# Performance work log

Hardware: AMD Instinct MI355X
Metric: run time of the kernel (lower is better)

The kernel has to match this reference:

```python
import jax, jax.numpy as jnp
import numpy as np

D_MODEL = 1024
N_HEADS = 16
D_HEAD = 64
NEG = -1000000000.0


def setup_inputs() -> dict:
    key = jax.random.key(0)
    k1, k2, k3 = jax.random.split(key, 3)
    B, T = 2, 2048
    x = jax.random.normal(k1, (B, T, D_MODEL), dtype=jnp.float32)
    # qkv_proj: Linear(d_model, 3*H*D, bias=False) -> weight (3*H*D, d_model)
    w_qkv = jax.random.normal(k2, (3 * N_HEADS * D_HEAD, D_MODEL), dtype=jnp.float32) * (D_MODEL ** -0.5)
    # o_proj: Linear(H*D, d_model, bias=False) -> weight (d_model, H*D)
    w_o = jax.random.normal(k3, (D_MODEL, N_HEADS * D_HEAD), dtype=jnp.float32) * ((N_HEADS * D_HEAD) ** -0.5)
    return {"x": x, "w_qkv": w_qkv, "w_o": w_o}


def reference(x, w_qkv, w_o):
    B, T, _ = x.shape
    H, D = N_HEADS, D_HEAD
    scale = D ** -0.5
    qkv = jnp.einsum('btm,nm->btn', x, w_qkv).reshape(B, T, 3, H, D)
    q, k, v = qkv[:, :, 0], qkv[:, :, 1], qkv[:, :, 2]  # (B,T,H,D)
    # scores: (B,H,T,T)
    attn = jnp.einsum('bqhd,bkhd->bhqk', q, k) * scale
    causal = jnp.tril(jnp.ones((T, T), dtype=x.dtype))
    attn = attn + (1.0 - causal) * NEG
    attn = jax.nn.softmax(attn, axis=-1)
    out = jnp.einsum('bhqk,bkhd->bqhd', attn, v).reshape(B, T, H * D)
    out = jnp.einsum('btn,mn->btm', out, w_o)
    return (out, k, v)
```

## Files before the change

kernel.cpp:

```cpp
#include <hip/hip_runtime.h>
#include <cstdint>

typedef unsigned short u16;
typedef __bf16 bf16x8 __attribute__((ext_vector_type(8)));
typedef float f32x4 __attribute__((ext_vector_type(4)));
typedef short s4 __attribute__((ext_vector_type(4)));

#define T_SEQ 2048
#define NH 16

__device__ __forceinline__ u16 f2bf(float f) {
  union { float f; uint32_t u; } x; x.f = f;
  uint32_t r = (x.u + 0x7fffu + ((x.u >> 16) & 1u)) >> 16;
  return (u16)r;
}

__device__ __forceinline__ uint32_t pk2bf(float a, float b) {
  union { float f; uint32_t u; } x, y; x.f = a; y.f = b;
  uint32_t lo = (x.u + 0x7fffu + ((x.u >> 16) & 1u)) >> 16;
  uint32_t hi = (y.u + 0x7fffu + ((y.u >> 16) & 1u)) >> 16;
  return lo | (hi << 16);
}

__device__ __forceinline__ void cvt8(u16* dst, const float* src) {
  float4 a = *(const float4*)src;
  float4 b = *(const float4*)(src + 4);
  uint4 o;
  o.x = pk2bf(a.x, a.y); o.y = pk2bf(a.z, a.w);
  o.z = pk2bf(b.x, b.y); o.w = pk2bf(b.z, b.w);
  *(uint4*)dst = o;
}

__global__ __launch_bounds__(256) void cvt_all(const float* __restrict__ x,
                                               const float* __restrict__ wq,
                                               const float* __restrict__ wo,
                                               u16* __restrict__ dst) {
  int i = blockIdx.x * 256 + threadIdx.x;
  const float* src; int off;
  if (i < 524288)      { src = x;  off = 0; }
  else if (i < 917504) { src = wq; off = 524288; }
  else                 { src = wo; off = 917504; }
  cvt8(&dst[(size_t)i * 8], &src[(size_t)(i - off) * 8]);
}

__device__ __forceinline__ s4 cvt4(f32x4 v) {
  union { __bf16 b[4]; s4 s; } u;
  u.b[0] = (__bf16)v[0]; u.b[1] = (__bf16)v[1];
  u.b[2] = (__bf16)v[2]; u.b[3] = (__bf16)v[3];
  return u.s;
}

__device__ __forceinline__ f32x4 mfma16(s4 a, s4 b, f32x4 c) {
#if __has_builtin(__builtin_amdgcn_mfma_f32_16x16x16bf16_1k)
  return __builtin_amdgcn_mfma_f32_16x16x16bf16_1k(a, b, c, 0, 0, 0);
#else
  asm("v_mfma_f32_16x16x16_bf16 %0, %1, %2, %0" : "+v"(c) : "v"(a), "v"(b));
  return c;
#endif
}

__device__ __forceinline__ float exp2fast(float x) {
#if __has_builtin(__builtin_amdgcn_exp2f)
  return __builtin_amdgcn_exp2f(x);
#else
  float r; asm("v_exp_f32 %0, %1" : "=v"(r) : "v"(x)); return r;
#endif
}

__device__ __forceinline__ void gl_lds(const u16* g, u16* ldsbase) {
  __builtin_amdgcn_global_load_lds(
      (const __attribute__((address_space(1))) void*)g,
      (__attribute__((address_space(3))) void*)ldsbase, 16, 0, 0);
}

template <bool CF32, bool KV, int BM>
__global__ __launch_bounds__(512) void gemm_bt(
    const u16* __restrict__ A, const u16* __restrict__ W,
    void* __restrict__ Cp, float* __restrict__ outk, float* __restrict__ outv,
    u16* __restrict__ vtp, int M, int N, int K) {
  constexpr int WM = BM / 2;
  constexpr int MI = WM / 16;
  constexpr int NJ = 2;
  __shared__ __align__(16) u16 As[2][BM * 64];
  __shared__ __align__(16) u16 Bs[2][128 * 64];
  const int tid  = threadIdx.x;
  const int bid  = blockIdx.y * gridDim.x + blockIdx.x;
  const int per  = (gridDim.x * gridDim.y) >> 3;
  const int swz  = (bid & 7) * per + (bid >> 3);
  const int n0   = (swz % gridDim.x) * 128;
  const int m0   = (swz / gridDim.x) * BM;
  const int lane = tid & 63;
  const int wave = tid >> 6;
  const int wm   = (wave >> 2) * WM;
  const int wn   = (wave & 3) * 32;
  const int l15  = lane & 15;
  const int quad = lane >> 4;
  const int srow = lane >> 3;
  const int sc   = lane & 7;

  f32x4 acc[MI][NJ];
#pragma unroll
  for (int i = 0; i < MI; i++)
#pragma unroll
    for (int j = 0; j < NJ; j++) acc[i][j] = (f32x4){0.f, 0.f, 0.f, 0.f};

  auto stage = [&](int d, int k0) {
#pragma unroll
    for (int i = 0; i < BM / 64; i++) {
      int r0  = (i * 8 + wave) * 8;
      int row = r0 + srow;
      int gc  = (sc ^ (row & 7)) << 3;
      gl_lds(&A[(size_t)(m0 + row) * K + k0 + gc], &As[d][r0 * 64]);
    }
#pragma unroll
    for (int i = 0; i < 2; i++) {
      int r0  = (i * 8 + wave) * 8;
      int row = r0 + srow;
      int gc  = (sc ^ (row & 7)) << 3;
      gl_lds(&W[(size_t)(n0 + row) * K + k0 + gc], &Bs[d][r0 * 64]);
    }
  };

  stage(0, 0);
  asm volatile("s_waitcnt vmcnt(0)" ::: "memory");
  __builtin_amdgcn_s_barrier();
  __builtin_amdgcn_sched_barrier(0);

  const int NT = K >> 6;
  int cur = 0;
  for (int t = 0; t < NT; t++) {
    if (t + 1 < NT) stage(cur ^ 1, (t + 1) * 64);
#pragma unroll
    for (int kk = 0; kk < 64; kk += 32) {
      bf16x8 af[MI], bfr[NJ];
#pragma unroll
      for (int i = 0; i < MI; i++) {
        int arow = wm + i * 16 + l15;
        af[i] = *(const bf16x8*)((const char*)&As[cur][0] + arow * 128 +
                                 ((((kk >> 3) + quad) ^ (arow & 7)) << 4));
      }
#pragma unroll
      for (int j = 0; j < NJ; j++) {
        int brow = wn + j * 16 + l15;
        bfr[j] = *(const bf16x8*)((const char*)&Bs[cur][0] + brow * 128 +
                                  ((((kk >> 3) + quad) ^ (brow & 7)) << 4));
      }
#pragma unroll
      for (int i = 0; i < MI; i++)
#pragma unroll
        for (int j = 0; j < NJ; j++)
          acc[i][j] = __builtin_amdgcn_mfma_f32_16x16x32_bf16(af[i], bfr[j], acc[i][j], 0, 0, 0);
    }
    asm volatile("s_waitcnt vmcnt(0)" ::: "memory");
    __builtin_amdgcn_s_barrier();
    __builtin_amdgcn_sched_barrier(0);
    cur ^= 1;
  }
#pragma unroll
  for (int i = 0; i < MI; i++)
#pragma unroll
    for (int j = 0; j < NJ; j++) {
      const int row0 = m0 + wm + i * 16 + quad * 4;
      const int col  = n0 + wn + j * 16 + l15;
      if constexpr (CF32) {
#pragma unroll
        for (int r = 0; r < 4; r++)
          ((float*)Cp)[(size_t)(row0 + r) * N + col] = acc[i][j][r];
      } else if (KV && col >= 2048) {
        const int hd = col - 2048;
        const int b_ = row0 >> 11, t_ = row0 & 2047;
        uint2 pk;
        pk.x = pk2bf(acc[i][j][0], acc[i][j][1]);
        pk.y = pk2bf(acc[i][j][2], acc[i][j][3]);
        *(uint2*)&vtp[((size_t)(b_ * NH + (hd >> 6)) * 64 + (hd & 63)) * 2048 + t_] = pk;
#pragma unroll
        for (int r = 0; r < 4; r++)
          outv[(size_t)(row0 + r) * 1024 + hd] = acc[i][j][r];
      } else {
#pragma unroll
        for (int r = 0; r < 4; r++) {
          float v = acc[i][j][r];
          ((u16*)Cp)[(size_t)(row0 + r) * N + col] = f2bf(v);
          if constexpr (KV) {
            if (col >= 1024) outk[(size_t)(row0 + r) * 1024 + (col - 1024)] = v;
          }
        }
      }
    }
}

__global__ __launch_bounds__(256) void attn(const u16* __restrict__ qkv,
                                            const u16* __restrict__ vt,
                                            u16* __restrict__ o) {
  __shared__ __align__(16) u16 Ks[2][64 * 64];
  __shared__ __align__(16) u16 Vts[2][64 * 64];

  const int tid  = threadIdx.x;
  const int bx   = blockIdx.x;
  const int by   = blockIdx.y;
  const int b    = by >> 4, h = by & 15;
  const int lane = tid & 63, wave = tid >> 6;
  const int l15  = lane & 15, quad = lane >> 4;
  const int srow = lane >> 3, sc = lane & 7;
  const size_t qbase = (size_t)b * T_SEQ * 3072;
  const size_t vbase = (size_t)(b * NH + h) * 64 * 2048;
  const float C = 0.1803368801f;

  const int u  = (bx + (by & 7) * 5) & 31;
  const int c  = by >> 3;
  const int v_ = (u + ((c >> 1) << 4)) & 31;
  const int qt = (c & 1) ? (31 - v_) : v_;
  const int steps = qt + 1;

  const int wq0  = qt * 64 + wave * 16;
  const int qrow = wq0 + l15;

  const u16* qp = &qkv[qbase + (size_t)qrow * 3072 + h * 64];
  const bf16x8 qf0 = *(const bf16x8*)&qp[quad * 8];
  const bf16x8 qf1 = *(const bf16x8*)&qp[32 + quad * 8];

  f32x4 acc_o[4];
#pragma unroll
  for (int n = 0; n < 4; n++) acc_o[n] = (f32x4){0.f, 0.f, 0.f, 0.f};
  float m2run = -1e30f, lrun = 0.f;

  auto stage = [&](int buf, int kt) {
    const int k0 = kt * 64;
#pragma unroll
    for (int i = 0; i < 2; i++) {
      int r0  = (wave * 2 + i) * 8;
      int row = r0 + srow;
      int gc  = (sc ^ (row & 7)) << 3;
      gl_lds(&qkv[qbase + (size_t)(k0 + row) * 3072 + 1024 + h * 64 + gc], &Ks[buf][r0 * 64]);
      gl_lds(&vt[vbase + (size_t)row * 2048 + k0 + gc], &Vts[buf][r0 * 64]);
    }
  };

  stage(0, 0);

  for (int s = 0; s < steps; s++) {
    const int cur = s & 1;
    asm volatile("s_waitcnt vmcnt(0)" ::: "memory");
    __builtin_amdgcn_s_barrier();
    __builtin_amdgcn_sched_barrier(0);

    if (s + 1 < steps) stage(cur ^ 1, s + 1);

    const int k0 = s * 64;

    f32x4 sacc[4];
#pragma unroll
    for (int j = 0; j < 4; j++) sacc[j] = (f32x4){0.f, 0.f, 0.f, 0.f};
    __builtin_amdgcn_s_setprio(1);
#pragma unroll
    for (int j = 0; j < 4; j++) {
      int krow = j * 16 + l15;
      const char* kb = (const char*)&Ks[cur][0] + krow * 128;
      bf16x8 kfa = *(const bf16x8*)(kb + ((quad ^ (krow & 7)) << 4));
      bf16x8 kfb = *(const bf16x8*)(kb + (((4 + quad) ^ (krow & 7)) << 4));
      sacc[j] = __builtin_amdgcn_mfma_f32_16x16x32_bf16(kfa, qf0, sacc[j], 0, 0, 0);
      sacc[j] = __builtin_amdgcn_mfma_f32_16x16x32_bf16(kfb, qf1, sacc[j], 0, 0, 0);
    }
    __builtin_amdgcn_s_setprio(0);

    if (s == qt) {
#pragma unroll
      for (int j = 0; j < 4; j++)
#pragma unroll
        for (int r = 0; r < 4; r++) {
          int k = k0 + j * 16 + quad * 4 + r;
          if (k > qrow) sacc[j][r] = -1e30f;
        }
    }

    float mj[4];
#pragma unroll
    for (int j = 0; j < 4; j++)
      mj[j] = fmaxf(fmaxf(sacc[j][0], sacc[j][1]), fmaxf(sacc[j][2], sacc[j][3]));
    float mx = fmaxf(fmaxf(mj[0], mj[1]), fmaxf(mj[2], mj[3]));
    mx = fmaxf(mx, __shfl_xor(mx, 16));
    mx = fmaxf(mx, __shfl_xor(mx, 32));
    const float m2x = mx * C;

    if (!__all(m2x <= m2run + 8.0f)) {
      const float m2new = fmaxf(m2run, m2x);
      const float alpha = exp2fast(m2run - m2new);
      lrun *= alpha;
      m2run = m2new;
#pragma unroll
      for (int r = 0; r < 4; r++) {
        float ar = __shfl(alpha, quad * 4 + r);
#pragma unroll
        for (int n = 0; n < 4; n++) acc_o[n][r] *= ar;
      }
    }

    const float nm = m2run;
    float ts[4];
#pragma unroll
    for (int j = 0; j < 4; j++) {
#pragma unroll
      for (int r = 0; r < 4; r++) sacc[j][r] = exp2fast(fmaf(sacc[j][r], C, -nm));
      ts[j] = (sacc[j][0] + sacc[j][1]) + (sacc[j][2] + sacc[j][3]);
    }
    float sum = (ts[0] + ts[1]) + (ts[2] + ts[3]);
    sum += __shfl_xor(sum, 16);
    sum += __shfl_xor(sum, 32);
    lrun += sum;

    s4 pa[4];
#pragma unroll
    for (int j = 0; j < 4; j++) pa[j] = cvt4(sacc[j]);

    __builtin_amdgcn_s_setprio(1);
#pragma unroll
    for (int j = 0; j < 4; j++)
#pragma unroll
      for (int n = 0; n < 4; n++) {
        int vrow = n * 16 + l15;
        int ch = (j * 2 + (quad >> 1)) ^ (vrow & 7);
        const s4 vf = *(const s4*)((const char*)&Vts[cur][0] + vrow * 128 +
                                   (ch << 4) + ((quad & 1) << 3));
        acc_o[n] = mfma16(pa[j], vf, acc_o[n]);
      }
    __builtin_amdgcn_s_setprio(0);
  }

  const float linv = 1.0f / lrun;
#pragma unroll
  for (int r = 0; r < 4; r++) {
    const float lr = __shfl(linv, quad * 4 + r);
    const int row = wq0 + quad * 4 + r;
#pragma unroll
    for (int n = 0; n < 4; n++)
      o[(size_t)(b * T_SEQ + row) * 1024 + h * 64 + n * 16 + l15] =
          f2bf(acc_o[n][r] * lr);
  }
}

extern "C" void kernel_launch(void* const* d_in, const int* in_sizes, int n_in,
                              void* d_out, int out_size, void* d_ws, size_t ws_size,
                              hipStream_t stream) {
  const float* x     = (const float*)d_in[0];
  const float* w_qkv = (const float*)d_in[1];
  const float* w_o   = (const float*)d_in[2];
  float* out  = (float*)d_out;
  float* outk = out + (size_t)4194304;
  float* outv = out + (size_t)8388608;

  u16* qkv = (u16*)d_ws;
  u16* vt  = qkv + (size_t)4096 * 3072;
  u16* ao  = vt  + (size_t)4194304;
  u16* xb  = ao  + (size_t)4194304;
  u16* wqb = xb  + (size_t)4194304;
  u16* wob = wqb + (size_t)3145728;

  cvt_all<<<4096, 256, 0, stream>>>(x, w_qkv, w_o, xb);

  gemm_bt<false, true, 128><<<dim3(24, 32), 512, 0, stream>>>(
      xb, wqb, qkv, outk, outv, vt, 4096, 3072, 1024);
  attn<<<dim3(32, 32), 256, 0, stream>>>(qkv, vt, ao);
  gemm_bt<true, false, 64><<<dim3(8, 64), 512, 0, stream>>>(
      ao, wob, out, nullptr, nullptr, nullptr, 4096, 1024, 1024);
}
```

Baseline: 192.9 us.

## Split causal attention KV loop across two blocks by tile parity and merge

Each query tile with qt>=1 is now processed by two blocks, one handling even KV tiles and one odd, doubling the grid to 63x32. Each block writes an unnormalized bf16 partial output plus running max and sum into scratch reused from the output buffer and the xb workspace. A new merge kernel combines the two partials with softmax rescaling. This aims to shorten the longest per-block critical path and improve load balance and occupancy, at the cost of an extra kernel launch, extra global traffic, and bf16 rounding of the partials.

After: 202.6 us. 5.0% more time.

```diff
diff --git a/kernel.cpp b/kernel.cpp
--- a/kernel.cpp
+++ b/kernel.cpp
@@ -8,11 +8,19 @@
 
 #define T_SEQ 2048
 #define NH 16
+#define P_TILES 992
+#define P_O_U16 (P_TILES * 4096)
+#define P_ML_OFF_F 2031616
+#define P_ML 128
 
 __device__ __forceinline__ u16 f2bf(float f) {
   union { float f; uint32_t u; } x; x.f = f;
   uint32_t r = (x.u + 0x7fffu + ((x.u >> 16) & 1u)) >> 16;
   return (u16)r;
+}
+
+__device__ __forceinline__ float bf2f(u16 b) {
+  union { uint32_t u; float f; } x; x.u = ((uint32_t)b) << 16; return x.f;
 }
 
 __device__ __forceinline__ uint32_t pk2bf(float a, float b) {
@@ -191,7 +199,9 @@
 
 __global__ __launch_bounds__(256) void attn(const u16* __restrict__ qkv,
                                             const u16* __restrict__ vt,
-                                            u16* __restrict__ o) {
+                                            u16* __restrict__ o,
+                                            u16* __restrict__ poA,
+                                            u16* __restrict__ poB) {
   __shared__ __align__(16) u16 Ks[2][64 * 64];
   __shared__ __align__(16) u16 Vts[2][64 * 64];
 
@@ -206,11 +216,11 @@
   const size_t vbase = (size_t)(b * NH + h) * 64 * 2048;
   const float C = 0.1803368801f;
 
-  const int u  = (bx + (by & 7) * 5) & 31;
-  const int c  = by >> 3;
-  const int v_ = (u + ((c >> 1) << 4)) & 31;
-  const int qt = (c & 1) ? (31 - v_) : v_;
-  const int steps = qt + 1;
+  int qt, parity;
+  if (bx == 62) { qt = 0; parity = 0; }
+  else          { qt = 31 - (bx >> 1); parity = bx & 1; }
+  const int nsteps = (parity == 0) ? (qt / 2 + 1) : ((qt + 1) / 2);
+  const bool split = (qt >= 1);
 
   const int wq0  = qt * 64 + wave * 16;
   const int qrow = wq0 + l15;
@@ -236,17 +246,18 @@
     }
   };
 
-  stage(0, 0);
-
-  for (int s = 0; s < steps; s++) {
+  stage(0, parity);
+
+  for (int s = 0; s < nsteps; s++) {
     const int cur = s & 1;
+    const int kt  = parity + 2 * s;
     asm volatile("s_waitcnt vmcnt(0)" ::: "memory");
     __builtin_amdgcn_s_barrier();
     __builtin_amdgcn_sched_barrier(0);
 
-    if (s + 1 < steps) stage(cur ^ 1, s + 1);
-
-    const int k0 = s * 64;
+    if (s + 1 < nsteps) stage(cur ^ 1, parity + 2 * (s + 1));
+
+    const int k0 = kt * 64;
 
     f32x4 sacc[4];
 #pragma unroll
@@ -263,7 +274,7 @@
     }
     __builtin_amdgcn_s_setprio(0);
 
-    if (s == qt) {
+    if (kt == qt) {
 #pragma unroll
       for (int j = 0; j < 4; j++)
 #pragma unroll
@@ -326,16 +337,73 @@
     __builtin_amdgcn_s_setprio(0);
   }
 
-  const float linv = 1.0f / lrun;
-#pragma unroll
-  for (int r = 0; r < 4; r++) {
-    const float lr = __shfl(linv, quad * 4 + r);
-    const int row = wq0 + quad * 4 + r;
-#pragma unroll
-    for (int n = 0; n < 4; n++)
-      o[(size_t)(b * T_SEQ + row) * 1024 + h * 64 + n * 16 + l15] =
-          f2bf(acc_o[n][r] * lr);
+  if (split) {
+    const int t = by * 31 + (qt - 1);
+    u16* po   = (parity == 0) ? poA : poB;
+    float* ml = (float*)((parity == 0) ? poA : poB) + P_ML_OFF_F;
+    u16* PO   = po + (size_t)t * 4096;
+    float* ML = ml + (size_t)t * P_ML;
+#pragma unroll
+    for (int r = 0; r < 4; r++) {
+      int row = wave * 16 + quad * 4 + r;
+#pragma unroll
+      for (int n = 0; n < 4; n++)
+        PO[row * 64 + n * 16 + l15] = f2bf(acc_o[n][r]);
+    }
+    if (quad == 0) {
+      int row = wave * 16 + l15;
+      ML[row * 2]     = m2run;
+      ML[row * 2 + 1] = lrun;
+    }
+  } else {
+    const float linv = 1.0f / lrun;
+#pragma unroll
+    for (int r = 0; r < 4; r++) {
+      const float lr = __shfl(linv, quad * 4 + r);
+      const int row = wq0 + quad * 4 + r;
+#pragma unroll
+      for (int n = 0; n < 4; n++)
+        o[(size_t)(b * T_SEQ + row) * 1024 + h * 64 + n * 16 + l15] =
+            f2bf(acc_o[n][r] * lr);
+    }
   }
+}
+
+__global__ __launch_bounds__(256) void merge_attn(const u16* __restrict__ poA,
+                                                  const u16* __restrict__ poB,
+                                                  u16* __restrict__ ao) {
+  const int qt = blockIdx.x + 1;
+  const int by = blockIdx.y;
+  const int b  = by >> 4, h = by & 15;
+  const int t  = by * 31 + (qt - 1);
+  const int tid = threadIdx.x;
+  const int row = tid >> 2;
+  const int cg  = (tid & 3) * 16;
+  const u16* POA = poA + (size_t)t * 4096 + row * 64 + cg;
+  const u16* POB = poB + (size_t)t * 4096 + row * 64 + cg;
+  const float* MLA = (const float*)poA + P_ML_OFF_F + (size_t)t * P_ML + row * 2;
+  const float* MLB = (const float*)poB + P_ML_OFF_F + (size_t)t * P_ML + row * 2;
+  const float mA = MLA[0], lA = MLA[1];
+  const float mB = MLB[0], lB = MLB[1];
+  const float m  = fmaxf(mA, mB);
+  const float sA = exp2fast(mA - m), sB = exp2fast(mB - m);
+  const float inv = 1.0f / (lA * sA + lB * sB);
+  const float fA = sA * inv, fB = sB * inv;
+  union { uint4 v[2]; u16 s[16]; } A, B;
+  A.v[0] = *(const uint4*)POA;  A.v[1] = *(const uint4*)(POA + 8);
+  B.v[0] = *(const uint4*)POB;  B.v[1] = *(const uint4*)(POB + 8);
+  float c[16];
+#pragma unroll
+  for (int k = 0; k < 16; k++)
+    c[k] = bf2f(A.s[k]) * fA + bf2f(B.s[k]) * fB;
+  uint4 o0, o1;
+  o0.x = pk2bf(c[0], c[1]);   o0.y = pk2bf(c[2], c[3]);
+  o0.z = pk2bf(c[4], c[5]);   o0.w = pk2bf(c[6], c[7]);
+  o1.x = pk2bf(c[8], c[9]);   o1.y = pk2bf(c[10], c[11]);
+  o1.z = pk2bf(c[12], c[13]); o1.w = pk2bf(c[14], c[15]);
+  u16* dst = &ao[((size_t)(b * T_SEQ + qt * 64 + row)) * 1024 + h * 64 + cg];
+  *(uint4*)dst = o0;
+  *(uint4*)(dst + 8) = o1;
 }
 
 extern "C" void kernel_launch(void* const* d_in, const int* in_sizes, int n_in,
@@ -355,11 +423,15 @@
   u16* wqb = xb  + (size_t)4194304;
   u16* wob = wqb + (size_t)3145728;
 
+  u16* poA = (u16*)out;
+  u16* poB = xb;
+
   cvt_all<<<4096, 256, 0, stream>>>(x, w_qkv, w_o, xb);
 
   gemm_bt<false, true, 128><<<dim3(24, 32), 512, 0, stream>>>(
       xb, wqb, qkv, outk, outv, vt, 4096, 3072, 1024);
-  attn<<<dim3(32, 32), 256, 0, stream>>>(qkv, vt, ao);
+  attn<<<dim3(63, 32), 256, 0, stream>>>(qkv, vt, ao, poA, poB);
+  merge_attn<<<dim3(31, 32), 256, 0, stream>>>(poA, poB, ao);
   gemm_bt<true, false, 64><<<dim3(8, 64), 512, 0, stream>>>(
       ao, wob, out, nullptr, nullptr, nullptr, 4096, 1024, 1024);
 }
```

## Switch GEMM to three-stage LDS pipeline with K=32 tiles and MFMA priority

Applied to the files above, without the earlier changes.

Replaces the double-buffered K=64 staging in the projection GEMM with a triple-buffered K=32 ring. Loads run two tiles ahead, with partial vmcnt waits so only the current tile must have landed before the single barrier. The XOR swizzle is changed to a 4-chunk pattern, and s_setprio is raised around the MFMA block. The intent is to hide global-to-LDS latency better and drop one barrier per step, at the cost of more loop iterations and a finer-grained sync.

Result: no change. 190.9 us (-1.0%).

```diff
diff --git a/kernel.cpp b/kernel.cpp
--- a/kernel.cpp
+++ b/kernel.cpp
@@ -81,8 +81,8 @@
   constexpr int WM = BM / 2;
   constexpr int MI = WM / 16;
   constexpr int NJ = 2;
-  __shared__ __align__(16) u16 As[2][BM * 64];
-  __shared__ __align__(16) u16 Bs[2][128 * 64];
+  __shared__ __align__(16) u16 As[3][BM * 32];
+  __shared__ __align__(16) u16 Bs[3][128 * 32];
   const int tid  = threadIdx.x;
   const int bid  = blockIdx.y * gridDim.x + blockIdx.x;
   const int per  = (gridDim.x * gridDim.y) >> 3;
@@ -95,8 +95,9 @@
   const int wn   = (wave & 3) * 32;
   const int l15  = lane & 15;
   const int quad = lane >> 4;
-  const int srow = lane >> 3;
-  const int sc   = lane & 7;
+  const int srow = lane >> 2;
+  const int sc   = lane & 3;
+  const bool ldA = (BM == 128) || (wave < 4);
 
   f32x4 acc[MI][NJ];
 #pragma unroll
@@ -104,58 +105,58 @@
 #pragma unroll
     for (int j = 0; j < NJ; j++) acc[i][j] = (f32x4){0.f, 0.f, 0.f, 0.f};
 
-  auto stage = [&](int d, int k0) {
-#pragma unroll
-    for (int i = 0; i < BM / 64; i++) {
-      int r0  = (i * 8 + wave) * 8;
-      int row = r0 + srow;
-      int gc  = (sc ^ (row & 7)) << 3;
-      gl_lds(&A[(size_t)(m0 + row) * K + k0 + gc], &As[d][r0 * 64]);
-    }
-#pragma unroll
-    for (int i = 0; i < 2; i++) {
-      int r0  = (i * 8 + wave) * 8;
-      int row = r0 + srow;
-      int gc  = (sc ^ (row & 7)) << 3;
-      gl_lds(&W[(size_t)(n0 + row) * K + k0 + gc], &Bs[d][r0 * 64]);
+  auto stage = [&](int buf, int k0) {
+    {
+      int r0 = wave * 16, row = r0 + srow;
+      int gc = (sc ^ (row & 3)) << 3;
+      gl_lds(&W[(size_t)(n0 + row) * K + k0 + gc], &Bs[buf][r0 * 32]);
+    }
+    if (ldA) {
+      int r0 = wave * 16, row = r0 + srow;
+      int gc = (sc ^ (row & 3)) << 3;
+      gl_lds(&A[(size_t)(m0 + row) * K + k0 + gc], &As[buf][r0 * 32]);
     }
   };
 
   stage(0, 0);
-  asm volatile("s_waitcnt vmcnt(0)" ::: "memory");
-  __builtin_amdgcn_s_barrier();
-  __builtin_amdgcn_sched_barrier(0);
-
-  const int NT = K >> 6;
-  int cur = 0;
+  stage(1, 32);
+
+  const int NT = K >> 5;
   for (int t = 0; t < NT; t++) {
-    if (t + 1 < NT) stage(cur ^ 1, (t + 1) * 64);
-#pragma unroll
-    for (int kk = 0; kk < 64; kk += 32) {
-      bf16x8 af[MI], bfr[NJ];
-#pragma unroll
-      for (int i = 0; i < MI; i++) {
-        int arow = wm + i * 16 + l15;
-        af[i] = *(const bf16x8*)((const char*)&As[cur][0] + arow * 128 +
-                                 ((((kk >> 3) + quad) ^ (arow & 7)) << 4));
-      }
-#pragma unroll
-      for (int j = 0; j < NJ; j++) {
-        int brow = wn + j * 16 + l15;
-        bfr[j] = *(const bf16x8*)((const char*)&Bs[cur][0] + brow * 128 +
-                                  ((((kk >> 3) + quad) ^ (brow & 7)) << 4));
-      }
-#pragma unroll
-      for (int i = 0; i < MI; i++)
-#pragma unroll
-        for (int j = 0; j < NJ; j++)
-          acc[i][j] = __builtin_amdgcn_mfma_f32_16x16x32_bf16(af[i], bfr[j], acc[i][j], 0, 0, 0);
-    }
-    asm volatile("s_waitcnt vmcnt(0)" ::: "memory");
+    const int cur = t % 3;
+    if (t + 1 < NT) {
+      if (ldA) asm volatile("s_waitcnt vmcnt(2)" ::: "memory");
+      else     asm volatile("s_waitcnt vmcnt(1)" ::: "memory");
+    } else {
+      asm volatile("s_waitcnt vmcnt(0)" ::: "memory");
+    }
     __builtin_amdgcn_s_barrier();
     __builtin_amdgcn_sched_barrier(0);
-    cur ^= 1;
+
+    if (t + 2 < NT) stage((t + 2) % 3, (t + 2) * 32);
+
+    bf16x8 af[MI], bfr[NJ];
+#pragma unroll
+    for (int i = 0; i < MI; i++) {
+      int arow = wm + i * 16 + l15;
+      af[i] = *(const bf16x8*)((const char*)&As[cur][0] + arow * 64 +
+                               ((quad ^ (arow & 3)) << 4));
+    }
+#pragma unroll
+    for (int j = 0; j < NJ; j++) {
+      int brow = wn + j * 16 + l15;
+      bfr[j] = *(const bf16x8*)((const char*)&Bs[cur][0] + brow * 64 +
+                                ((quad ^ (brow & 3)) << 4));
+    }
+    __builtin_amdgcn_s_setprio(1);
+#pragma unroll
+    for (int i = 0; i < MI; i++)
+#pragma unroll
+      for (int j = 0; j < NJ; j++)
+        acc[i][j] = __builtin_amdgcn_mfma_f32_16x16x32_bf16(af[i], bfr[j], acc[i][j], 0, 0, 0);
+    __builtin_amdgcn_s_setprio(0);
   }
+
 #pragma unroll
   for (int i = 0; i < MI; i++)
 #pragma unroll
```
